# Performance work log

Hardware: AMD Instinct MI355X
Metric: run time of the kernel (lower is better)

Reference implementation:

```python
import jax, jax.numpy as jnp
import numpy as np
import math

N_FREQ = 10
N_FRAGMENTS = 4_000_000
CELL_N = 2000
GENE_N = 1000
EMB_DIM = N_FREQ * 2 * 2  # 40


def setup_inputs() -> dict:
    key = jax.random.key(0)
    k1, k2, k3, k4 = jax.random.split(key, 4)
    coords = jax.random.normal(k1, (N_FRAGMENTS, 2), dtype=jnp.float32)
    ix = jnp.sort(jax.random.randint(k2, (N_FRAGMENTS,), 0, CELL_N * GENE_N, dtype=jnp.int32))
    # buffers, exactly as in FragmentEmbedder.__init__
    freqs = np.array([[1.0 / 100.0 ** (2.0 * i / N_FREQ)] * 2 for i in range(1, N_FREQ + 1)],
                     dtype=np.float32).reshape(-1)  # [2*n_freq]
    shifts = np.array([[0.0, math.pi / 2.0] for _ in range(1, N_FREQ + 1)],
                      dtype=np.float32).reshape(-1)  # [2*n_freq]
    # params (weight1 is zero-init in the original; use small random so output is non-trivial)
    weight1 = jax.random.normal(k3, (1, EMB_DIM), dtype=jnp.float32) * 0.02
    bias1 = jax.random.normal(k4, (GENE_N,), dtype=jnp.float32)  # mean_gene_expression
    return {
        "fragment_coordinates": coords,
        "fragment_cellxgene_ix": ix,
        "cell_n": CELL_N,
        "gene_n": GENE_N,
        "gene_ix": jnp.arange(GENE_N, dtype=jnp.int32),
        "frequencies": jnp.asarray(freqs),
        "shifts": jnp.asarray(shifts),
        "weight1": weight1,
        "bias1": bias1,
    }


def reference(fragment_coordinates, fragment_cellxgene_ix, cell_n, gene_n, gene_ix,
              frequencies, shifts, weight1, bias1):
    F = fragment_coordinates.shape[0]
    # sinusoidal fragment embedding: [F, 2, 2*n_freq] -> [F, 4*n_freq]
    emb = jnp.sin(fragment_coordinates[..., None] * frequencies + shifts).reshape(F, -1)
    # sorted segment sum into cell x gene buckets
    pooled = jax.ops.segment_sum(emb, fragment_cellxgene_ix,
                                 num_segments=cell_n * gene_n,
                                 indices_are_sorted=True)
    cell_gene_embedding = pooled.reshape(cell_n, gene_n, emb.shape[-1])
    # einsum 'abc,bc->ab' with weight1 of shape (1, C) == contraction over C only
    expression = jnp.einsum("abc,c->ab", cell_gene_embedding, weight1[0]) + bias1[gene_ix]
    return expression
```

## Files before the change

### kernel.cpp

```cpp
#include <hip/hip_runtime.h>
#include <math.h>

#define NFREQ 10
#define INV2PI 0.15915494309189535f
#define TPB 256
#define SCALE_F 1048576.0f
#define INV_SCALE 9.5367431640625e-07f

__global__ void coeff_kernel(const float* __restrict__ freqs,
                             const float* __restrict__ weight,
                             float* __restrict__ cbuf) {
    int i = threadIdx.x;
    if (i < NFREQ) {
        cbuf[i] = freqs[2 * i] * INV2PI;
#pragma unroll
        for (int c = 0; c < 2; ++c) {
            float A = weight[c * 2 * NFREQ + 2 * i];
            float B = weight[c * 2 * NFREQ + 2 * i + 1];
            cbuf[(1 + 2 * c) * NFREQ + i] = sqrtf(A * A + B * B);
            cbuf[(2 + 2 * c) * NFREQ + i] = atan2f(B, A) * INV2PI;
        }
    }
}

__global__ __launch_bounds__(256) void zero_kernel(int* __restrict__ acc, int total) {
    int t = blockIdx.x * blockDim.x + threadIdx.x;
    int b = t * 4;
    if (b + 3 < total) {
        *(int4*)(acc + b) = make_int4(0, 0, 0, 0);
    } else {
        for (int k = 0; k < 4; ++k)
            if (b + k < total) acc[b + k] = 0;
    }
}

__device__ __forceinline__ float frag_scalar(
        float x, float y,
        const float* __restrict__ fr,
        const float* __restrict__ R0, const float* __restrict__ P0,
        const float* __restrict__ R1, const float* __restrict__ P1) {
    float sa = 0.f, sb = 0.f;
#pragma unroll
    for (int i = 0; i < NFREQ; ++i) {
        sa += R0[i] * __builtin_amdgcn_sinf(x * fr[i] + P0[i]);
        sb += R1[i] * __builtin_amdgcn_sinf(y * fr[i] + P1[i]);
    }
    return sa + sb;
}

__global__ __launch_bounds__(TPB) void scan_kernel(
        const float* __restrict__ coords,
        const int*   __restrict__ ix,
        const float* __restrict__ cbuf,
        int* __restrict__ acc,
        int F) {
    float fr[NFREQ], R0[NFREQ], P0[NFREQ], R1[NFREQ], P1[NFREQ];
#pragma unroll
    for (int i = 0; i < NFREQ; ++i) {
        fr[i] = cbuf[i];
        R0[i] = cbuf[NFREQ + i];
        P0[i] = cbuf[2 * NFREQ + i];
        R1[i] = cbuf[3 * NFREQ + i];
        P1[i] = cbuf[4 * NFREQ + i];
    }

    const long long f = (long long)blockIdx.x * TPB + threadIdx.x;
    const int lane = threadIdx.x & 63;
    const bool valid = (f < F);

    int   key = -2;
    float s   = 0.0f;
    if (valid) {
        key = ix[f];
        float2 c = *(const float2*)(coords + 2 * f);
        s = frag_scalar(c.x, c.y, fr, R0, P0, R1, P1);
    }

    float v = s;
#pragma unroll
    for (int d = 1; d < 64; d <<= 1) {
        float ov = __shfl_down(v, d);
        int   ok = __shfl_down(key, d);
        if (lane + d < 64 && ok == key) v += ov;
    }

    const int upkey = __shfl_up(key, 1);
    const bool head = valid && (lane == 0 || key != upkey);
    if (head)
        atomicAdd(acc + key, __float2int_rn(v * SCALE_F));
}

__global__ __launch_bounds__(256) void finish_kernel(
        float* out, const float* __restrict__ bias,
        const int* __restrict__ gix, int gene_n, int total) {
    int b = (blockIdx.x * blockDim.x + threadIdx.x) * 4;
    if ((gene_n & 3) == 0 && b + 3 < total) {
        int4 a = *(const int4*)((const int*)out + b);
        int g = b % gene_n;
        float4 r;
        r.x = bias[gix[g]]     + (float)a.x * INV_SCALE;
        r.y = bias[gix[g + 1]] + (float)a.y * INV_SCALE;
        r.z = bias[gix[g + 2]] + (float)a.z * INV_SCALE;
        r.w = bias[gix[g + 3]] + (float)a.w * INV_SCALE;
        *(float4*)(out + b) = r;
    } else {
        for (int k = 0; k < 4; ++k) {
            int j = b + k;
            if (j < total) {
                int aj = ((const int*)out)[j];
                out[j] = bias[gix[j % gene_n]] + (float)aj * INV_SCALE;
            }
        }
    }
}

extern "C" void kernel_launch(void* const* d_in, const int* in_sizes, int n_in,
                              void* d_out, int out_size, void* d_ws, size_t ws_size,
                              hipStream_t stream) {
    const float* coords  = (const float*)d_in[0];
    const int*   ix      = (const int*)d_in[1];
    const int*   gene_ix = (const int*)d_in[4];
    const float* freqs   = (const float*)d_in[5];
    const float* weight  = (const float*)d_in[7];
    const float* bias    = (const float*)d_in[8];
    float* out = (float*)d_out;

    int F      = in_sizes[1];
    int gene_n = in_sizes[4];
    int total  = out_size;

    float* cbuf = (float*)d_ws;

    hipLaunchKernelGGL(coeff_kernel, dim3(1), dim3(64), 0, stream,
                       freqs, weight, cbuf);

    int zthreads = (total + 3) / 4;
    hipLaunchKernelGGL(zero_kernel, dim3((zthreads + 255) / 256), dim3(256),
                       0, stream, (int*)out, total);

    int blocks = (int)(((long long)F + TPB - 1) / TPB);
    hipLaunchKernelGGL(scan_kernel, dim3(blocks), dim3(TPB), 0, stream,
                       coords, ix, cbuf, (int*)out, F);

    hipLaunchKernelGGL(finish_kernel, dim3((zthreads + 255) / 256), dim3(256),
                       0, stream, out, bias, gene_ix, gene_n, total);
}
```

Baseline: 115.7 us.

## Process two fragments per thread, merge coeff and zero kernels, pack sin math

Each scan thread now handles two adjacent fragments using vectorized int2/float4 loads. It pre-combines the pair when both share a key and fixes up the segmented reduction across the pair boundary. The coefficient computation is folded into the zeroing kernel and stored in device globals, which removes one launch and the workspace buffer. The sin accumulation uses two-wide vector types that may map to packed FP32 ops. The trade-off is extra edge-case logic and a possible second atomic per thread at segment boundaries.

```diff
diff --git a/kernel.cpp b/kernel.cpp
--- a/kernel.cpp
+++ b/kernel.cpp
@@ -4,28 +4,30 @@
 #define NFREQ 10
 #define INV2PI 0.15915494309189535f
 #define TPB 256
+#define FPT 2
 #define SCALE_F 1048576.0f
 #define INV_SCALE 9.5367431640625e-07f
 
-__global__ void coeff_kernel(const float* __restrict__ freqs,
-                             const float* __restrict__ weight,
-                             float* __restrict__ cbuf) {
-    int i = threadIdx.x;
-    if (i < NFREQ) {
-        cbuf[i] = freqs[2 * i] * INV2PI;
-#pragma unroll
-        for (int c = 0; c < 2; ++c) {
-            float A = weight[c * 2 * NFREQ + 2 * i];
-            float B = weight[c * 2 * NFREQ + 2 * i + 1];
-            cbuf[(1 + 2 * c) * NFREQ + i] = sqrtf(A * A + B * B);
-            cbuf[(2 + 2 * c) * NFREQ + i] = atan2f(B, A) * INV2PI;
-        }
+typedef float v2f __attribute__((ext_vector_type(2)));
+
+__device__ float g_fr[NFREQ];
+__device__ v2f   g_P[NFREQ];
+__device__ v2f   g_R[NFREQ];
+
+__device__ __forceinline__ v2f mkv2(float a, float b) { v2f r; r.x = a; r.y = b; return r; }
+
+__global__ __launch_bounds__(256) void init_kernel(int* __restrict__ acc, int total,
+                                                   const float* __restrict__ freqs,
+                                                   const float* __restrict__ weight) {
+    if (blockIdx.x == 0 && threadIdx.x < NFREQ) {
+        int i = threadIdx.x;
+        g_fr[i] = freqs[2 * i] * INV2PI;
+        float A0 = weight[2 * i],             B0 = weight[2 * i + 1];
+        float A1 = weight[2 * NFREQ + 2 * i], B1 = weight[2 * NFREQ + 2 * i + 1];
+        g_R[i] = mkv2(sqrtf(A0 * A0 + B0 * B0), sqrtf(A1 * A1 + B1 * B1));
+        g_P[i] = mkv2(atan2f(B0, A0) * INV2PI, atan2f(B1, A1) * INV2PI);
     }
-}
-
-__global__ __launch_bounds__(256) void zero_kernel(int* __restrict__ acc, int total) {
-    int t = blockIdx.x * blockDim.x + threadIdx.x;
-    int b = t * 4;
+    int b = (blockIdx.x * blockDim.x + threadIdx.x) * 4;
     if (b + 3 < total) {
         *(int4*)(acc + b) = make_int4(0, 0, 0, 0);
     } else {
@@ -34,60 +36,72 @@
     }
 }
 
-__device__ __forceinline__ float frag_scalar(
-        float x, float y,
-        const float* __restrict__ fr,
-        const float* __restrict__ R0, const float* __restrict__ P0,
-        const float* __restrict__ R1, const float* __restrict__ P1) {
-    float sa = 0.f, sb = 0.f;
+__device__ __forceinline__ float frag_eval(v2f c, const float* __restrict__ fr,
+                                           const v2f* __restrict__ P,
+                                           const v2f* __restrict__ R) {
+    v2f acc = mkv2(0.f, 0.f);
 #pragma unroll
     for (int i = 0; i < NFREQ; ++i) {
-        sa += R0[i] * __builtin_amdgcn_sinf(x * fr[i] + P0[i]);
-        sb += R1[i] * __builtin_amdgcn_sinf(y * fr[i] + P1[i]);
+        v2f th = c * fr[i] + P[i];
+        v2f s;
+        s.x = __builtin_amdgcn_sinf(th.x);
+        s.y = __builtin_amdgcn_sinf(th.y);
+        acc += R[i] * s;
     }
-    return sa + sb;
+    return acc.x + acc.y;
 }
 
 __global__ __launch_bounds__(TPB) void scan_kernel(
         const float* __restrict__ coords,
         const int*   __restrict__ ix,
-        const float* __restrict__ cbuf,
         int* __restrict__ acc,
         int F) {
-    float fr[NFREQ], R0[NFREQ], P0[NFREQ], R1[NFREQ], P1[NFREQ];
+    float fr[NFREQ]; v2f P[NFREQ], R[NFREQ];
 #pragma unroll
     for (int i = 0; i < NFREQ; ++i) {
-        fr[i] = cbuf[i];
-        R0[i] = cbuf[NFREQ + i];
-        P0[i] = cbuf[2 * NFREQ + i];
-        R1[i] = cbuf[3 * NFREQ + i];
-        P1[i] = cbuf[4 * NFREQ + i];
+        fr[i] = g_fr[i]; P[i] = g_P[i]; R[i] = g_R[i];
     }
 
-    const long long f = (long long)blockIdx.x * TPB + threadIdx.x;
+    const int t  = blockIdx.x * TPB + threadIdx.x;
+    const int f0 = 2 * t;
     const int lane = threadIdx.x & 63;
-    const bool valid = (f < F);
 
-    int   key = -2;
-    float s   = 0.0f;
-    if (valid) {
-        key = ix[f];
-        float2 c = *(const float2*)(coords + 2 * f);
-        s = frag_scalar(c.x, c.y, fr, R0, P0, R1, P1);
+    int   ka = -2, kb = -3;
+    float sa = 0.f, sb = 0.f;
+    if (f0 + 1 < F) {
+        int2   k2 = *(const int2*)(ix + f0);
+        float4 c4 = *(const float4*)(coords + 2 * f0);
+        ka = k2.x; kb = k2.y;
+        sa = frag_eval(mkv2(c4.x, c4.y), fr, P, R);
+        sb = frag_eval(mkv2(c4.z, c4.w), fr, P, R);
+    } else if (f0 < F) {
+        ka = ix[f0];
+        float2 c2 = *(const float2*)(coords + 2 * f0);
+        sa = frag_eval(mkv2(c2.x, c2.y), fr, P, R);
     }
 
-    float v = s;
+    const bool pure = (ka == kb);
+    float v = pure ? (sa + sb) : sa;
+
 #pragma unroll
     for (int d = 1; d < 64; d <<= 1) {
         float ov = __shfl_down(v, d);
-        int   ok = __shfl_down(key, d);
-        if (lane + d < 64 && ok == key) v += ov;
+        int   ok = __shfl_down(ka, d);
+        if (lane + d < 64 && ok == ka) v += ov;
     }
 
-    const int upkey = __shfl_up(key, 1);
-    const bool head = valid && (lane == 0 || key != upkey);
-    if (head)
-        atomicAdd(acc + key, __float2int_rn(v * SCALE_F));
+    const float nv  = __shfl_down(v, 1);
+    const int   nk  = __shfl_down(ka, 1);
+    const int   pkb = __shfl_up(kb, 1);
+
+    const bool headA = (ka >= 0) && (lane == 0 || ka != pkb);
+    if (headA)
+        atomicAdd(acc + ka, __float2int_rn(v * SCALE_F));
+
+    if (kb >= 0 && !pure) {
+        float tb = sb + ((lane < 63 && nk == kb) ? nv : 0.f);
+        atomicAdd(acc + kb, __float2int_rn(tb * SCALE_F));
+    }
 }
 
 __global__ __launch_bounds__(256) void finish_kernel(
@@ -129,18 +143,15 @@
     int gene_n = in_sizes[4];
     int total  = out_size;
 
-    float* cbuf = (float*)d_ws;
-
-    hipLaunchKernelGGL(coeff_kernel, dim3(1), dim3(64), 0, stream,
-                       freqs, weight, cbuf);
+    (void)d_ws; (void)ws_size; (void)n_in;
 
     int zthreads = (total + 3) / 4;
-    hipLaunchKernelGGL(zero_kernel, dim3((zthreads + 255) / 256), dim3(256),
-                       0, stream, (int*)out, total);
+    hipLaunchKernelGGL(init_kernel, dim3((zthreads + 255) / 256), dim3(256),
+                       0, stream, (int*)out, total, freqs, weight);
 
-    int blocks = (int)(((long long)F + TPB - 1) / TPB);
+    int blocks = (F + TPB * FPT - 1) / (TPB * FPT);
     hipLaunchKernelGGL(scan_kernel, dim3(blocks), dim3(TPB), 0, stream,
-                       coords, ix, cbuf, (int*)out, F);
+                       coords, ix, (int*)out, F);
 
     hipLaunchKernelGGL(finish_kernel, dim3((zthreads + 255) / 256), dim3(256),
                        0, stream, out, bias, gene_ix, gene_n, total);
```

Result: faster. 110.5 us (-4.5%).
